# Optimization experiments

Measured on AMD Instinct MI355X. Metric: run time of the kernel, lower is better.

## Reference

```python
import jax, jax.numpy as jnp
import numpy as np

B, S, HID, LAYERS, HEADS, WINDOW = 2, 4096, 768, 4, 12, 256
W = WINDOW // 2            # one-sided window: each token attends to W left, W right
HD = HID // HEADS          # head dim = 64
MAXPOS = (S // WINDOW + 1) * WINDOW + 1
EPS = 1e-12                # Longformer layer_norm_eps


def layer_norm(x, g, b):
    m = x.mean(-1, keepdims=True)
    v = ((x - m) ** 2).mean(-1, keepdims=True)
    return (x - m) * jax.lax.rsqrt(v + EPS) * g + b


def sliding_window_attention(q, k, v, key_mask):
    # q,k,v: [B,H,S,D]; key_mask: [B,S] bool. Band attention: |i-j| <= W.
    Bz, Hh, Sl, D = q.shape
    nC = Sl // W
    q = q / jnp.sqrt(jnp.asarray(D, q.dtype))
    cidx = jnp.arange(nC)[:, None] + jnp.arange(3)[None, :]            # [nC,3] chunk gather
    kp = jnp.pad(k, ((0, 0), (0, 0), (W, W), (0, 0))).reshape(Bz, Hh, nC + 2, W, D)
    vp = jnp.pad(v, ((0, 0), (0, 0), (W, W), (0, 0))).reshape(Bz, Hh, nC + 2, W, D)
    kw = kp[:, :, cidx].reshape(Bz, Hh, nC, 3 * W, D)                  # keys for each query chunk
    vw = vp[:, :, cidx].reshape(Bz, Hh, nC, 3 * W, D)
    qc = q.reshape(Bz, Hh, nC, W, D)
    scores = jnp.einsum('bhcqd,bhckd->bhcqk', qc, kw)                  # [B,H,nC,W,3W]
    p = jnp.arange(W)[:, None]
    j = jnp.arange(3 * W)[None, :]
    band = (j >= p) & (j <= p + 2 * W)                                  # [W,3W] banded validity
    keypos = jnp.arange(nC)[:, None, None] * W + j[None] - W           # [nC,1,3W] global key idx
    inrange = (keypos >= 0) & (keypos < Sl)
    kmw = jnp.pad(key_mask, ((0, 0), (W, W))).reshape(Bz, nC + 2, W)[:, cidx].reshape(Bz, nC, 3 * W)
    mask = (band[None] & inrange)[None, None] & kmw[:, None, :, None, :]
    scores = jnp.where(mask, scores, jnp.asarray(-1e9, scores.dtype))
    probs = jax.nn.softmax(scores, axis=-1)
    out = jnp.einsum('bhcqk,bhckd->bhcqd', probs, vw)
    return out.reshape(Bz, Hh, Sl, D)


def heads_split(x):
    return x.reshape(x.shape[0], x.shape[1], HEADS, HD).transpose(0, 2, 1, 3)


def heads_merge(x):
    return x.transpose(0, 2, 1, 3).reshape(x.shape[0], x.shape[2], HID)


def forward(embeddings, pos_emb, tok_emb, emb_ln_g, emb_ln_b, Wq, bq, Wk, bk, Wv, bv,
            Wo, bo, ln1_g, ln1_b, Wi, bi, Wf, bf, ln2_g, ln2_b, Wp, bp, attention_mask):
    Sl = embeddings.shape[1]
    # Longformer embeddings: inputs_embeds + absolute positions (padding_idx+1 .. ) + token type 0
    h = embeddings + pos_emb[1:Sl + 1][None] + tok_emb[0][None, None]
    h = layer_norm(h, emb_ln_g, emb_ln_b)
    km = attention_mask.astype(bool)
    for l in range(LAYERS):
        q = heads_split(h @ Wq[l] + bq[l])
        k = heads_split(h @ Wk[l] + bk[l])
        v = heads_split(h @ Wv[l] + bv[l])
        a = heads_merge(sliding_window_attention(q, k, v, km))
        h = layer_norm(h + (a @ Wo[l] + bo[l]), ln1_g[l], ln1_b[l])
        f = jax.nn.gelu(h @ Wi[l] + bi[l], approximate=False) @ Wf[l] + bf[l]
        h = layer_norm(h + f, ln2_g[l], ln2_b[l])
    return jax.nn.sigmoid((h @ Wp + bp).squeeze(-1))


def setup_inputs() -> dict:
    key = jax.random.key(0)
    ks = jax.random.split(key, 12)
    nrm = lambda k, sh: jax.random.normal(k, sh, jnp.float32) * 0.02
    return dict(
        embeddings=jax.random.normal(ks[0], (B, S, HID), jnp.float32),
        attention_mask=jnp.ones((B, S), jnp.int32),
        pos_emb=nrm(ks[1], (MAXPOS, HID)),
        tok_emb=nrm(ks[2], (2, HID)),
        emb_ln_g=jnp.ones((HID,), jnp.float32),
        emb_ln_b=jnp.zeros((HID,), jnp.float32),
        Wq=nrm(ks[3], (LAYERS, HID, HID)), bq=jnp.zeros((LAYERS, HID), jnp.float32),
        Wk=nrm(ks[4], (LAYERS, HID, HID)), bk=jnp.zeros((LAYERS, HID), jnp.float32),
        Wv=nrm(ks[5], (LAYERS, HID, HID)), bv=jnp.zeros((LAYERS, HID), jnp.float32),
        Wo=nrm(ks[6], (LAYERS, HID, HID)), bo=jnp.zeros((LAYERS, HID), jnp.float32),
        ln1_g=jnp.ones((LAYERS, HID), jnp.float32), ln1_b=jnp.zeros((LAYERS, HID), jnp.float32),
        Wi=nrm(ks[7], (LAYERS, HID, 4 * HID)), bi=jnp.zeros((LAYERS, 4 * HID), jnp.float32),
        Wf=nrm(ks[8], (LAYERS, 4 * HID, HID)), bf=jnp.zeros((LAYERS, HID), jnp.float32),
        ln2_g=jnp.ones((LAYERS, HID), jnp.float32), ln2_b=jnp.zeros((LAYERS, HID), jnp.float32),
        Wp=nrm(ks[9], (HID, 1)), bp=jnp.zeros((1,), jnp.float32),
    )


def reference(embeddings, attention_mask, pos_emb, tok_emb, emb_ln_g, emb_ln_b, Wq, bq, Wk, bk,
              Wv, bv, Wo, bo, ln1_g, ln1_b, Wi, bi, Wf, bf, ln2_g, ln2_b, Wp, bp):
    return forward(embeddings, pos_emb, tok_emb, emb_ln_g, emb_ln_b, Wq, bq, Wk, bk, Wv, bv,
                   Wo, bo, ln1_g, ln1_b, Wi, bi, Wf, bf, ln2_g, ln2_b, Wp, bp, attention_mask)
```

## Files before the change

### kernel.cpp

```cpp
#include <hip/hip_runtime.h>
#include <hip/hip_bf16.h>


typedef __bf16 bf16;
typedef bf16  bf16x8  __attribute__((ext_vector_type(8)));
typedef float floatx4 __attribute__((ext_vector_type(4)));

#define MFMA16(a, b, c) __builtin_amdgcn_mfma_f32_16x16x32_bf16((a), (b), (c), 0, 0, 0)

__device__ __forceinline__ void gld_lds16(const bf16* gp, bf16* lp) {
  __builtin_amdgcn_global_load_lds(
      (const __attribute__((address_space(1))) void*)gp,
      (__attribute__((address_space(3))) void*)lp, 16, 0, 0);
}

__device__ __forceinline__ float fast_rcp(float x) {
  return __builtin_amdgcn_rcpf(x);
}

__device__ __forceinline__ float gelu_tanh(float v) {
  float t = 0.7978845608028654f * (v + 0.044715f * v * v * v);
  float e = __expf(2.f * t);
  float th = 1.f - 2.f * fast_rcp(e + 1.f);
  return 0.5f * v * (1.f + th);
}

static constexpr size_t SZ_WTQKV = (size_t)4 * 2304 * 768 * 2;
static constexpr size_t SZ_WTO   = (size_t)4 * 768 * 768 * 2;
static constexpr size_t SZ_WTI   = (size_t)4 * 3072 * 768 * 2;
static constexpr size_t SZ_WTF   = (size_t)4 * 768 * 3072 * 2;
static constexpr size_t SZ_BQKV  = (size_t)4 * 2304 * 4;
static constexpr size_t SZ_H32   = (size_t)8192 * 768 * 4;
static constexpr size_t SZ_HBF   = (size_t)8192 * 768 * 2;
static constexpr size_t SZ_QKV   = (size_t)8192 * 2304 * 2;
static constexpr size_t SZ_ATTN  = (size_t)8192 * 768 * 2;
static constexpr size_t SZ_TMP   = (size_t)8192 * 768 * 4;

static constexpr size_t OFF_WTQKV = 0;
static constexpr size_t OFF_WTO   = OFF_WTQKV + SZ_WTQKV;
static constexpr size_t OFF_WTI   = OFF_WTO   + SZ_WTO;
static constexpr size_t OFF_WTF   = OFF_WTI   + SZ_WTI;
static constexpr size_t OFF_BQKV  = OFF_WTF   + SZ_WTF;
static constexpr size_t OFF_H32   = OFF_BQKV  + SZ_BQKV;
static constexpr size_t OFF_HBF   = OFF_H32   + SZ_H32;
static constexpr size_t OFF_QKV   = OFF_HBF   + SZ_HBF;
static constexpr size_t OFF_ATTN  = OFF_QKV   + SZ_QKV;
static constexpr size_t OFF_TMP   = OFF_ATTN  + SZ_ATTN;
static constexpr size_t OFF_FFN1  = OFF_TMP   + SZ_TMP;

__global__ __launch_bounds__(256) void transpose_cast(
    const float* __restrict__ src, bf16* __restrict__ dst,
    int K, int N, long sStride, long dStride) {
  __shared__ float tile[32][33];
  const int l = blockIdx.z;
  src += (long)l * sStride;
  dst += (long)l * dStride;
  const int n0 = blockIdx.x * 32, k0 = blockIdx.y * 32;
  const int tx = threadIdx.x, ty = threadIdx.y;
#pragma unroll
  for (int i = 0; i < 4; ++i)
    tile[ty + i * 8][tx] = src[(long)(k0 + ty + i * 8) * N + n0 + tx];
  __syncthreads();
#pragma unroll
  for (int i = 0; i < 4; ++i)
    dst[(long)(n0 + ty + i * 8) * K + k0 + tx] = (bf16)tile[tx][ty + i * 8];
}

__global__ void bias_concat(const float* __restrict__ bq, const float* __restrict__ bk,
                            const float* __restrict__ bv, float* __restrict__ bqkv) {
  int i = blockIdx.x * 256 + threadIdx.x;
  if (i >= 4 * 2304) return;
  int l = i / 2304, p = i % 2304;
  float v = (p < 768) ? bq[l * 768 + p]
          : (p < 1536) ? bk[l * 768 + p - 768] : bv[l * 768 + p - 1536];
  bqkv[i] = v;
}

__device__ __forceinline__ void block_stats(float s1, float s2, float* red,
                                            float& mean, float& inv) {
  const int lane = threadIdx.x & 63, wave = threadIdx.x >> 6;
#pragma unroll
  for (int off = 32; off > 0; off >>= 1) {
    s1 += __shfl_down(s1, off, 64);
    s2 += __shfl_down(s2, off, 64);
  }
  if (lane == 0) { red[wave] = s1; red[4 + wave] = s2; }
  __syncthreads();
  s1 = red[0] + red[1] + red[2] + red[3];
  s2 = red[4] + red[5] + red[6] + red[7];
  mean = s1 * (1.f / 768.f);
  float var = s2 * (1.f / 768.f) - mean * mean;
  inv = rsqrtf(var + 1e-12f);
}

__global__ __launch_bounds__(256) void embed_ln_kernel(
    const float* __restrict__ emb, const float* __restrict__ pos,
    const float* __restrict__ tok, const float* __restrict__ g,
    const float* __restrict__ bta, float* __restrict__ h32, bf16* __restrict__ hbf) {
  __shared__ float red[8];
  const long base = (long)blockIdx.x * 768;
  const int s = blockIdx.x & 4095;
  const int t = threadIdx.x;
  float x[3], s1 = 0.f, s2 = 0.f;
#pragma unroll
  for (int i = 0; i < 3; ++i) {
    int c = t + i * 256;
    float v = emb[base + c] + pos[(long)(s + 1) * 768 + c] + tok[c];
    x[i] = v; s1 += v; s2 += v * v;
  }
  float mean, inv;
  block_stats(s1, s2, red, mean, inv);
#pragma unroll
  for (int i = 0; i < 3; ++i) {
    int c = t + i * 256;
    float y = (x[i] - mean) * inv * g[c] + bta[c];
    h32[base + c] = y;
    hbf[base + c] = (bf16)y;
  }
}

__global__ __launch_bounds__(256) void add_ln_kernel(
    float* __restrict__ h32, const float* __restrict__ p0,
    const float* __restrict__ p1, const float* __restrict__ bias,
    const float* __restrict__ g, const float* __restrict__ bta,
    bf16* __restrict__ hbf) {
  __shared__ float red[8];
  const long base = (long)blockIdx.x * 768;
  const int t = threadIdx.x;
  float x[3], s1 = 0.f, s2 = 0.f;
#pragma unroll
  for (int i = 0; i < 3; ++i) {
    int c = t + i * 256;
    float v = h32[base + c] + p0[base + c] + p1[base + c] + bias[c];
    x[i] = v; s1 += v; s2 += v * v;
  }
  float mean, inv;
  block_stats(s1, s2, red, mean, inv);
#pragma unroll
  for (int i = 0; i < 3; ++i) {
    int c = t + i * 256;
    float y = (x[i] - mean) * inv * g[c] + bta[c];
    h32[base + c] = y;
    hbf[base + c] = (bf16)y;
  }
}

template <int MODE>
__global__ __launch_bounds__(256) void gemm_kernel(
    const bf16* __restrict__ A, const bf16* __restrict__ BT,
    const float* __restrict__ bias, void* __restrict__ C0, void* __restrict__ C1,
    int N, int ld, int ksize) {
  __shared__ bf16 As[128 * 64];
  __shared__ bf16 Bs[128 * 64];
  const int tid  = threadIdx.x;
  const int wave = tid >> 6, lane = tid & 63, l15 = lane & 15, quad = lane >> 4;
  const int wm = wave >> 1, wn = wave & 1;
  const long m0 = (long)blockIdx.x * 128;
  const int  n0 = blockIdx.y * 128;
  const int  k0 = blockIdx.z * ksize;

  floatx4 acc[4][4] = {};
  const bf16* Ag = A + m0 * ld + k0;
  const bf16* Bg = BT + (long)n0 * ld + k0;
  const int rowoff = tid >> 3;
  const int sc_sw = (tid & 7) ^ (rowoff & 7);
  const int fsw = l15 & 7;

  for (int kt = 0; kt < ksize; kt += 64) {
#pragma unroll
    for (int p = 0; p < 4; ++p) {
      const int row = p * 32 + rowoff;
      gld_lds16(Ag + (long)row * ld + kt + sc_sw * 8, As + p * 2048 + wave * 512);
      gld_lds16(Bg + (long)row * ld + kt + sc_sw * 8, Bs + p * 2048 + wave * 512);
    }
    __syncthreads();
#pragma unroll
    for (int kk = 0; kk < 2; ++kk) {
      const int ch = ((kk * 4 + quad) ^ fsw) * 8;
      bf16x8 af[4], bfr[4];
#pragma unroll
      for (int mt = 0; mt < 4; ++mt)
        af[mt] = *(const bf16x8*)&As[(wm * 64 + mt * 16 + l15) * 64 + ch];
#pragma unroll
      for (int nt = 0; nt < 4; ++nt)
        bfr[nt] = *(const bf16x8*)&Bs[(wn * 64 + nt * 16 + l15) * 64 + ch];
#pragma unroll
      for (int mt = 0; mt < 4; ++mt)
#pragma unroll
        for (int nt = 0; nt < 4; ++nt)
          acc[mt][nt] = MFMA16(af[mt], bfr[nt], acc[mt][nt]);
    }
    __syncthreads();
  }

  float* Cp32 = (MODE == 0) ? ((blockIdx.z == 0) ? (float*)C0 : (float*)C1) : nullptr;
#pragma unroll
  for (int nt = 0; nt < 4; ++nt) {
    const int col = n0 + wn * 64 + nt * 16 + l15;
    const float bb = (MODE == 0) ? 0.f : bias[col];
#pragma unroll
    for (int mt = 0; mt < 4; ++mt) {
      const long row = m0 + wm * 64 + mt * 16 + quad * 4;
#pragma unroll
      for (int r = 0; r < 4; ++r) {
        float v = acc[mt][nt][r] + bb;
        if (MODE == 2) v = gelu_tanh(v);
        if (MODE == 0) Cp32[(row + r) * N + col] = v;
        else           ((bf16*)C0)[(row + r) * N + col] = (bf16)v;
      }
    }
  }
}

__global__ __launch_bounds__(256) void vtrans_kernel(
    const bf16* __restrict__ qkv, bf16* __restrict__ vt) {
  __shared__ bf16 tile[64 * 68];
  const int s0 = blockIdx.x * 64, h = blockIdx.y, b = blockIdx.z;
  const int tid = threadIdx.x;
  const bf16* src = qkv + (long)b * 4096 * 2304 + 1536 + h * 64;
#pragma unroll
  for (int p = 0; p < 2; ++p) {
    const int i = p * 256 + tid;
    const int r = i >> 3, c = i & 7;
    *(uint4*)&tile[r * 68 + c * 8] = *(const uint4*)&src[(long)(s0 + r) * 2304 + c * 8];
  }
  __syncthreads();
  bf16* dst = vt + ((long)(b * 12 + h)) * 64 * 4096;
#pragma unroll
  for (int p = 0; p < 2; ++p) {
    const int i = p * 256 + tid;
    const int d = i >> 3, cs = i & 7;
    bf16 vals[8];
#pragma unroll
    for (int u = 0; u < 8; ++u) vals[u] = tile[(cs * 8 + u) * 68 + d];
    *(uint4*)&dst[(long)d * 4096 + s0 + cs * 8] = *(const uint4*)vals;
  }
}

__global__ __launch_bounds__(256) void attn_kernel(
    const bf16* __restrict__ qkv, const bf16* __restrict__ vt,
    const int* __restrict__ amask, bf16* __restrict__ attn_out) {
  constexpr int S = 4096, HID3 = 2304;
  __shared__ bf16 Ss[64 * 328];
  __shared__ bf16 Ts[64 * 64];
  __shared__ float redm[64], reds[64];

  const int x = blockIdx.x, q0 = x * 64, h = blockIdx.y, b = blockIdx.z;
  const int tid = threadIdx.x, wave = tid >> 6, lane = tid & 63;
  const int l15 = lane & 15, quad = lane >> 4;
  const int rowoff = tid >> 3;
  const int sc_sw = (tid & 7) ^ (rowoff & 7);
  const int fsw = l15 & 7;
  const int t_lo = (x < 2) ? (2 - x) : 0;
  const int t_hi = (x > 61) ? (66 - x) : 5;

  const bf16* Qb = qkv + (long)b * S * HID3 + h * 64;
  const bf16* Kb = Qb + 768;
  const bf16* Vt_bh = vt + ((long)(b * 12 + h)) * 64 * 4096;

  bf16x8 qf[2];
  {
    const long qrow = q0 + wave * 16 + l15;
    qf[0] = *(const bf16x8*)&Qb[qrow * HID3 + quad * 8];
    qf[1] = *(const bf16x8*)&Qb[qrow * HID3 + 32 + quad * 8];
  }

  float mrow[4] = {-3e38f, -3e38f, -3e38f, -3e38f};

  for (int t = t_lo; t < t_hi; ++t) {
    const int j0 = (x - 2 + t) * 64;
    __syncthreads();
#pragma unroll
    for (int p = 0; p < 2; ++p) {
      const int key = p * 32 + rowoff;
      gld_lds16(Kb + (long)(j0 + key) * HID3 + sc_sw * 8, &Ts[p * 2048 + wave * 512]);
    }
    __syncthreads();
    floatx4 sacc[4] = {};
#pragma unroll
    for (int kk = 0; kk < 2; ++kk) {
      const int ch = ((kk * 4 + quad) ^ fsw) * 8;
#pragma unroll
      for (int nt = 0; nt < 4; ++nt) {
        bf16x8 kf = *(const bf16x8*)&Ts[(nt * 16 + l15) * 64 + ch];
        sacc[nt] = MFMA16(qf[kk], kf, sacc[nt]);
      }
    }
#pragma unroll
    for (int nt = 0; nt < 4; ++nt) {
      const int jj = t * 64 + nt * 16 + l15;
      const int j = j0 + nt * 16 + l15;
      const bool jv = (amask[b * S + j] != 0);
#pragma unroll
      for (int r = 0; r < 4; ++r) {
        const int qi = wave * 16 + quad * 4 + r;
        const bool ok = jv && (jj >= qi) && (jj <= qi + 256);
        const float sv = ok ? sacc[nt][r] * 0.125f : -1e9f;
        mrow[r] = fmaxf(mrow[r], sv);
        Ss[(wave * 16 + quad * 4 + r) * 328 + jj] = (bf16)sv;
      }
    }
  }
#pragma unroll
  for (int off = 1; off < 16; off <<= 1)
#pragma unroll
    for (int r = 0; r < 4; ++r)
      mrow[r] = fmaxf(mrow[r], __shfl_xor(mrow[r], off, 64));
  if (l15 == 0) {
#pragma unroll
    for (int r = 0; r < 4; ++r) redm[wave * 16 + quad * 4 + r] = mrow[r];
  }
  __syncthreads();

  {
    const int row = wave * 16 + l15;
    const float mx = redm[row];
    float sum = 0.f;
    for (int c = t_lo * 8 + quad; c < t_hi * 8; c += 4) {
      bf16x8 pv = *(const bf16x8*)&Ss[row * 328 + c * 8];
#pragma unroll
      for (int u = 0; u < 8; ++u) {
        const float p = __expf((float)pv[u] - mx);
        sum += p;
        pv[u] = (bf16)p;
      }
      *(bf16x8*)&Ss[row * 328 + c * 8] = pv;
    }
    sum += __shfl_xor(sum, 16, 64);
    sum += __shfl_xor(sum, 32, 64);
    if (quad == 0) reds[row] = sum;
  }
  __syncthreads();

  floatx4 oacc[4] = {};
  for (int t = t_lo; t < t_hi; ++t) {
    const int j0 = (x - 2 + t) * 64;
    __syncthreads();
#pragma unroll
    for (int p = 0; p < 2; ++p) {
      const int d = p * 32 + rowoff;
      gld_lds16(Vt_bh + (long)d * 4096 + j0 + sc_sw * 8, &Ts[p * 2048 + wave * 512]);
    }
    __syncthreads();
#pragma unroll
    for (int kk = 0; kk < 2; ++kk) {
      const int ko = kk * 32 + quad * 8;
      const int ch = ((kk * 4 + quad) ^ fsw) * 8;
      bf16x8 pf = *(const bf16x8*)&Ss[(wave * 16 + l15) * 328 + t * 64 + ko];
#pragma unroll
      for (int nt = 0; nt < 4; ++nt) {
        bf16x8 vf = *(const bf16x8*)&Ts[(nt * 16 + l15) * 64 + ch];
        oacc[nt] = MFMA16(pf, vf, oacc[nt]);
      }
    }
  }

  float inv[4];
#pragma unroll
  for (int r = 0; r < 4; ++r) inv[r] = fast_rcp(reds[wave * 16 + quad * 4 + r]);
  const long orow = (long)b * S + q0 + wave * 16 + quad * 4;
#pragma unroll
  for (int nt = 0; nt < 4; ++nt)
#pragma unroll
    for (int r = 0; r < 4; ++r)
      attn_out[(orow + r) * 768 + h * 64 + nt * 16 + l15] =
          (bf16)(oacc[nt][r] * inv[r]);
}

__global__ __launch_bounds__(256) void final_kernel(
    const float* __restrict__ h32, const float* __restrict__ Wp,
    const float* __restrict__ bp, float* __restrict__ out) {
  const int wave = threadIdx.x >> 6, lane = threadIdx.x & 63;
  const long tok = (long)blockIdx.x * 4 + wave;
  float s = 0.f;
#pragma unroll
  for (int i = 0; i < 12; ++i) {
    const int c = lane + i * 64;
    s += h32[tok * 768 + c] * Wp[c];
  }
#pragma unroll
  for (int off = 32; off > 0; off >>= 1) s += __shfl_down(s, off, 64);
  if (lane == 0) out[tok] = fast_rcp(1.f + __expf(-(s + bp[0])));
}

extern "C" void kernel_launch(void* const* d_in, const int* in_sizes, int n_in,
                              void* d_out, int out_size, void* d_ws, size_t ws_size,
                              hipStream_t stream) {
  const float* emb   = (const float*)d_in[0];
  const int*   amask = (const int*)d_in[1];
  const float* pos   = (const float*)d_in[2];
  const float* tok   = (const float*)d_in[3];
  const float* elng  = (const float*)d_in[4];
  const float* elnb  = (const float*)d_in[5];
  const float* Wq = (const float*)d_in[6];   const float* bq = (const float*)d_in[7];
  const float* Wk = (const float*)d_in[8];   const float* bk = (const float*)d_in[9];
  const float* Wv = (const float*)d_in[10];  const float* bv = (const float*)d_in[11];
  const float* Wo = (const float*)d_in[12];  const float* bo = (const float*)d_in[13];
  const float* ln1g = (const float*)d_in[14]; const float* ln1b = (const float*)d_in[15];
  const float* Wi = (const float*)d_in[16];  const float* bi = (const float*)d_in[17];
  const float* Wf = (const float*)d_in[18];  const float* bfb = (const float*)d_in[19];
  const float* ln2g = (const float*)d_in[20]; const float* ln2b = (const float*)d_in[21];
  const float* Wp = (const float*)d_in[22];  const float* bp = (const float*)d_in[23];
  float* out = (float*)d_out;

  char* ws = (char*)d_ws;
  bf16*  WTqkv = (bf16*)(ws + OFF_WTQKV);
  bf16*  WTo   = (bf16*)(ws + OFF_WTO);
  bf16*  WTi   = (bf16*)(ws + OFF_WTI);
  bf16*  WTf   = (bf16*)(ws + OFF_WTF);
  float* bqkv  = (float*)(ws + OFF_BQKV);
  float* h32   = (float*)(ws + OFF_H32);
  bf16*  hbf   = (bf16*)(ws + OFF_HBF);
  bf16*  qkvb  = (bf16*)(ws + OFF_QKV);
  float* part1 = (float*)(ws + OFF_QKV);
  bf16*  attnb = (bf16*)(ws + OFF_ATTN);
  float* tmp   = (float*)(ws + OFF_TMP);
  bf16*  vtb   = (bf16*)(ws + OFF_TMP);
  bf16*  ffn1  = (bf16*)(ws + OFF_FFN1);

  const dim3 tb(32, 8, 1);
  transpose_cast<<<dim3(24, 24, 4), tb, 0, stream>>>(Wq, WTqkv,               768, 768,  (long)768 * 768,  (long)2304 * 768);
  transpose_cast<<<dim3(24, 24, 4), tb, 0, stream>>>(Wk, WTqkv + 768 * 768,   768, 768,  (long)768 * 768,  (long)2304 * 768);
  transpose_cast<<<dim3(24, 24, 4), tb, 0, stream>>>(Wv, WTqkv + 1536 * 768,  768, 768,  (long)768 * 768,  (long)2304 * 768);
  transpose_cast<<<dim3(24, 24, 4), tb, 0, stream>>>(Wo, WTo,                 768, 768,  (long)768 * 768,  (long)768 * 768);
  transpose_cast<<<dim3(96, 24, 4), tb, 0, stream>>>(Wi, WTi,                 768, 3072, (long)768 * 3072, (long)3072 * 768);
  transpose_cast<<<dim3(24, 96, 4), tb, 0, stream>>>(Wf, WTf,                 3072, 768, (long)3072 * 768, (long)768 * 3072);
  bias_concat<<<36, 256, 0, stream>>>(bq, bk, bv, bqkv);

  embed_ln_kernel<<<8192, 256, 0, stream>>>(emb, pos, tok, elng, elnb, h32, hbf);

  for (int l = 0; l < 4; ++l) {
    gemm_kernel<1><<<dim3(64, 18, 1), 256, 0, stream>>>(
        hbf, WTqkv + (size_t)l * 2304 * 768, bqkv + l * 2304, qkvb, nullptr, 2304, 768, 768);
    vtrans_kernel<<<dim3(64, 12, 2), 256, 0, stream>>>(qkvb, vtb);
    attn_kernel<<<dim3(64, 12, 2), 256, 0, stream>>>(qkvb, vtb, amask, attnb);
    gemm_kernel<0><<<dim3(64, 6, 2), 256, 0, stream>>>(
        attnb, WTo + (size_t)l * 768 * 768, nullptr, tmp, part1, 768, 768, 384);
    add_ln_kernel<<<8192, 256, 0, stream>>>(h32, tmp, part1, bo + l * 768,
                                            ln1g + l * 768, ln1b + l * 768, hbf);
    gemm_kernel<2><<<dim3(64, 24, 1), 256, 0, stream>>>(
        hbf, WTi + (size_t)l * 3072 * 768, bi + l * 3072, ffn1, nullptr, 3072, 768, 768);
    gemm_kernel<0><<<dim3(64, 6, 2), 256, 0, stream>>>(
        ffn1, WTf + (size_t)l * 768 * 3072, nullptr, tmp, part1, 768, 3072, 1536);
    add_ln_kernel<<<8192, 256, 0, stream>>>(h32, tmp, part1, bfb + l * 768,
                                            ln2g + l * 768, ln2b + l * 768, hbf);
  }

  final_kernel<<<2048, 256, 0, stream>>>(h32, Wp, bp, out);
}
```

Before: 1.283 ms.

## Stage GEMM epilogue through LDS for vectorized stores; store split-K partials as bf16

The GEMM epilogue now writes each wave's 16x64 accumulator slice into LDS and then issues 16-byte vectorized global stores, replacing scattered 2- and 4-byte per-element stores. The split-K partial sums for the output and FFN-down projections are stored as bf16 instead of fp32, and add_ln reads them as bf16. This halves partial-sum traffic and improves store coalescing. The cost is lower precision in the residual partials and extra LDS round trips in the epilogue, which reuse the A tile buffer.

```diff
diff --git a/kernel.cpp b/kernel.cpp
--- a/kernel.cpp
+++ b/kernel.cpp
@@ -120,8 +120,8 @@
 }
 
 __global__ __launch_bounds__(256) void add_ln_kernel(
-    float* __restrict__ h32, const float* __restrict__ p0,
-    const float* __restrict__ p1, const float* __restrict__ bias,
+    float* __restrict__ h32, const bf16* __restrict__ p0,
+    const bf16* __restrict__ p1, const float* __restrict__ bias,
     const float* __restrict__ g, const float* __restrict__ bta,
     bf16* __restrict__ hbf) {
   __shared__ float red[8];
@@ -131,7 +131,7 @@
 #pragma unroll
   for (int i = 0; i < 3; ++i) {
     int c = t + i * 256;
-    float v = h32[base + c] + p0[base + c] + p1[base + c] + bias[c];
+    float v = h32[base + c] + (float)p0[base + c] + (float)p1[base + c] + bias[c];
     x[i] = v; s1 += v; s2 += v * v;
   }
   float mean, inv;
@@ -193,21 +193,26 @@
     __syncthreads();
   }
 
-  float* Cp32 = (MODE == 0) ? ((blockIdx.z == 0) ? (float*)C0 : (float*)C1) : nullptr;
-#pragma unroll
-  for (int nt = 0; nt < 4; ++nt) {
-    const int col = n0 + wn * 64 + nt * 16 + l15;
-    const float bb = (MODE == 0) ? 0.f : bias[col];
-#pragma unroll
-    for (int mt = 0; mt < 4; ++mt) {
-      const long row = m0 + wm * 64 + mt * 16 + quad * 4;
+  bf16* Cg = (bf16*)((MODE == 0 && blockIdx.z != 0) ? C1 : C0);
+  bf16* Es = As + wave * 1152;
+#pragma unroll
+  for (int mt = 0; mt < 4; ++mt) {
+#pragma unroll
+    for (int nt = 0; nt < 4; ++nt) {
+      const float bb = (MODE == 0) ? 0.f : bias[n0 + wn * 64 + nt * 16 + l15];
 #pragma unroll
       for (int r = 0; r < 4; ++r) {
         float v = acc[mt][nt][r] + bb;
         if (MODE == 2) v = gelu_tanh(v);
-        if (MODE == 0) Cp32[(row + r) * N + col] = v;
-        else           ((bf16*)C0)[(row + r) * N + col] = (bf16)v;
+        Es[(quad * 4 + r) * 72 + nt * 16 + l15] = (bf16)v;
       }
+    }
+#pragma unroll
+    for (int p = 0; p < 2; ++p) {
+      const int rr = p * 8 + (lane >> 3);
+      const int cc = (lane & 7) * 8;
+      bf16x8 vv = *(const bf16x8*)&Es[rr * 72 + cc];
+      *(bf16x8*)&Cg[(m0 + wm * 64 + mt * 16 + rr) * N + n0 + wn * 64 + cc] = vv;
     }
   }
 }
@@ -412,9 +417,9 @@
   float* h32   = (float*)(ws + OFF_H32);
   bf16*  hbf   = (bf16*)(ws + OFF_HBF);
   bf16*  qkvb  = (bf16*)(ws + OFF_QKV);
-  float* part1 = (float*)(ws + OFF_QKV);
+  bf16*  part1 = (bf16*)(ws + OFF_QKV);
   bf16*  attnb = (bf16*)(ws + OFF_ATTN);
-  float* tmp   = (float*)(ws + OFF_TMP);
+  bf16*  part0 = (bf16*)(ws + OFF_TMP);
   bf16*  vtb   = (bf16*)(ws + OFF_TMP);
   bf16*  ffn1  = (bf16*)(ws + OFF_FFN1);
 
@@ -435,14 +440,14 @@
     vtrans_kernel<<<dim3(64, 12, 2), 256, 0, stream>>>(qkvb, vtb);
     attn_kernel<<<dim3(64, 12, 2), 256, 0, stream>>>(qkvb, vtb, amask, attnb);
     gemm_kernel<0><<<dim3(64, 6, 2), 256, 0, stream>>>(
-        attnb, WTo + (size_t)l * 768 * 768, nullptr, tmp, part1, 768, 768, 384);
-    add_ln_kernel<<<8192, 256, 0, stream>>>(h32, tmp, part1, bo + l * 768,
+        attnb, WTo + (size_t)l * 768 * 768, nullptr, part0, part1, 768, 768, 384);
+    add_ln_kernel<<<8192, 256, 0, stream>>>(h32, part0, part1, bo + l * 768,
                                             ln1g + l * 768, ln1b + l * 768, hbf);
     gemm_kernel<2><<<dim3(64, 24, 1), 256, 0, stream>>>(
         hbf, WTi + (size_t)l * 3072 * 768, bi + l * 3072, ffn1, nullptr, 3072, 768, 768);
     gemm_kernel<0><<<dim3(64, 6, 2), 256, 0, stream>>>(
-        ffn1, WTf + (size_t)l * 768 * 3072, nullptr, tmp, part1, 768, 3072, 1536);
-    add_ln_kernel<<<8192, 256, 0, stream>>>(h32, tmp, part1, bfb + l * 768,
+        ffn1, WTf + (size_t)l * 768 * 3072, nullptr, part0, part1, 768, 3072, 1536);
+    add_ln_kernel<<<8192, 256, 0, stream>>>(h32, part0, part1, bfb + l * 768,
                                             ln2g + l * 768, ln2b + l * 768, hbf);
   }
 
```

Result: faster. 1.151 ms (-10.3%).
